# Performance work log

Hardware: AMD Instinct MI355X
Metric: run time of the kernel (lower is better)

The kernel has to match this reference:

```python
import jax, jax.numpy as jnp
from jax import lax
import numpy as np

N_QUBITS = 8
Q_DEPTH = 10
DIM = 256  # 2**8

# basis-state bit table; wire 0 = most-significant bit (PennyLane convention)
_bits = ((np.arange(DIM)[:, None] >> (N_QUBITS - 1 - np.arange(N_QUBITS))) & 1)
# phase layer: S on even wires (phase i), T on odd wires (phase e^{i pi/4})
_ph = np.where(np.arange(N_QUBITS) % 2 == 0, 1j, np.exp(1j * np.pi / 4))
_diag = np.prod(np.power(_ph[None, :], _bits), axis=1)
# entangling_layer_3 CZ pattern
_cz = np.ones(DIM)
for i, j in [(0, 1), (2, 3), (4, 5), (6, 7), (1, 2), (3, 4), (5, 6)]:
    _cz = _cz * ((-1.0) ** (_bits[:, i] * _bits[:, j]))
DIAG = jnp.asarray((_diag * _cz).astype(np.complex64))  # phase+CZ layer fused diagonal
ZSIGNS = jnp.asarray((1 - 2 * _bits).astype(np.float32))  # [256, 8] PauliZ eigenvalues
H_GATE = jnp.asarray((np.array([[1.0, 1.0], [1.0, -1.0]]) / np.sqrt(2.0)).astype(np.complex64))
X_GATE = jnp.asarray(np.array([[0.0, 1.0], [1.0, 0.0]]).astype(np.complex64))
EYE2 = jnp.eye(2, dtype=jnp.complex64)
BN_EPS = 1e-5


def apply_1q(state, U, w):
    """Apply 2x2 gate U on wire w; state: [B, 2,2,...,2]."""
    state = jnp.moveaxis(state, w + 1, -1)
    state = jnp.matmul(state, U.T)
    return jnp.moveaxis(state, -1, w + 1)


def quantum_net(features, q_params):
    """Batched statevector sim of quantum_net_3. features [B,256], q_params [80] -> [B,8]."""
    f = features / jnp.linalg.norm(features, axis=1, keepdims=True)
    state = f.astype(jnp.complex64).reshape((-1,) + (2,) * N_QUBITS)
    for w in range(N_QUBITS):
        state = apply_1q(state, H_GATE, w)
    qw = q_params.reshape(Q_DEPTH, N_QUBITS)
    for layer in range(Q_DEPTH):
        for w in range(N_QUBITS):
            t = qw[layer, w]
            c = jnp.cos(t / 2).astype(jnp.complex64)
            s = jnp.sin(t / 2).astype(jnp.complex64)
            U = c * EYE2 + (-1j) * s * X_GATE  # RX(t)
            state = apply_1q(state, U, w)
        flat = state.reshape(-1, DIM) * DIAG  # phase layer + CZ entangling (diagonal)
        state = flat.reshape((-1,) + (2,) * N_QUBITS)
    sv = state.reshape(-1, DIM)
    probs = sv.real ** 2 + sv.imag ** 2
    return probs @ ZSIGNS  # [B, 8] expval(PauliZ_i)


def conv2d(x, w, b):
    y = lax.conv_general_dilated(x, w, (1, 1), 'SAME', dimension_numbers=('NCHW', 'OIHW', 'NCHW'))
    return y + b[None, :, None, None]


def bn(x, gamma, beta, mean, var):  # eval-mode BatchNorm2d
    inv = gamma / jnp.sqrt(var + BN_EPS)
    return x * inv[None, :, None, None] + (beta - mean * inv)[None, :, None, None]


def maxpool2(x):
    return lax.reduce_window(x, -jnp.inf, lax.max, (1, 1, 2, 2), (1, 1, 2, 2), 'VALID')


def setup_inputs() -> dict:
    key = jax.random.key(0)
    ks = jax.random.split(key, 16)
    B = 1024
    return {
        'x': jax.random.normal(ks[0], (B, 1, 28, 28), dtype=jnp.float32),
        'conv1_w': 0.1 * jax.random.normal(ks[1], (32, 1, 3, 3), dtype=jnp.float32),
        'conv1_b': jnp.zeros((32,), jnp.float32),
        'bn1_gamma': jnp.ones((32,), jnp.float32),
        'bn1_beta': jnp.zeros((32,), jnp.float32),
        'bn1_mean': jnp.zeros((32,), jnp.float32),
        'bn1_var': jnp.ones((32,), jnp.float32),
        'conv2_w': 0.05 * jax.random.normal(ks[2], (64, 32, 3, 3), dtype=jnp.float32),
        'conv2_b': jnp.zeros((64,), jnp.float32),
        'bn2_gamma': jnp.ones((64,), jnp.float32),
        'bn2_beta': jnp.zeros((64,), jnp.float32),
        'bn2_mean': jnp.zeros((64,), jnp.float32),
        'bn2_var': jnp.ones((64,), jnp.float32),
        'fc_w': 0.01 * jax.random.normal(ks[3], (256, 64 * 7 * 7), dtype=jnp.float32),
        'fc_b': jnp.zeros((256,), jnp.float32),
        'q_params': 0.1 * jax.random.normal(ks[4], (Q_DEPTH * N_QUBITS,), dtype=jnp.float32),
        'p1_w': 0.01 * jax.random.normal(ks[5], (128, 8), dtype=jnp.float32),
        'p1_b': jnp.zeros((128,), jnp.float32),
        'p2_w': 0.01 * jax.random.normal(ks[6], (64, 128), dtype=jnp.float32),
        'p2_b': jnp.zeros((64,), jnp.float32),
        'p3_w': 0.01 * jax.random.normal(ks[7], (10, 64), dtype=jnp.float32),
        'p3_b': jnp.zeros((10,), jnp.float32),
    }


def reference(x, conv1_w, conv1_b, bn1_gamma, bn1_beta, bn1_mean, bn1_var,
              conv2_w, conv2_b, bn2_gamma, bn2_beta, bn2_mean, bn2_var,
              fc_w, fc_b, q_params, p1_w, p1_b, p2_w, p2_b, p3_w, p3_b):
    h = maxpool2(jax.nn.relu(bn(conv2d(x, conv1_w, conv1_b), bn1_gamma, bn1_beta, bn1_mean, bn1_var)))
    h = maxpool2(jax.nn.relu(bn(conv2d(h, conv2_w, conv2_b), bn2_gamma, bn2_beta, bn2_mean, bn2_var)))
    h = h.reshape(h.shape[0], -1)  # [B, 64*7*7]
    feats = jnp.tanh(h @ fc_w.T + fc_b)  # [B, 256]
    q = quantum_net(feats, q_params)  # [B, 8]
    z = jax.nn.relu(q @ p1_w.T + p1_b)  # dropout = identity (eval)
    z = jax.nn.relu(z @ p2_w.T + p2_b)
    return z @ p3_w.T + p3_b
```

## Files before the change

### kernel.cpp

```cpp
#include <hip/hip_runtime.h>
#include <math.h>


#define B_SZ 1024

#define OFF_FCWP   0
#define OFF_W2F    802816
#define OFF_W1T    821248
#define OFF_SC1    821536
#define OFF_SH1    821568
#define OFF_SC2    821600
#define OFF_SH2    821664
#define OFF_H1     821728
#define OFF_H2P    7244256

#define KSPLIT_FC 14
#define KCHUNK_FC 224

typedef __attribute__((ext_vector_type(8))) short s16x8;
typedef __attribute__((ext_vector_type(4))) float f32x4;

__constant__ float C_COS8[8] = {1.f, 0.70710678f, 0.f, -0.70710678f, -1.f, -0.70710678f, 0.f, 0.70710678f};
__constant__ float C_SIN8[8] = {0.f, 0.70710678f, 1.f, 0.70710678f, 0.f, -0.70710678f, -1.f, -0.70710678f};

__device__ __forceinline__ unsigned short bf16_rne(float f) {
  unsigned u = __float_as_uint(f);
  unsigned r = u + 0x7FFFu + ((u >> 16) & 1u);
  return (unsigned short)(r >> 16);
}
__device__ __forceinline__ int div14(int m) {
  return __float2int_rz((float)m * 0.07142858f);
}
__device__ __forceinline__ int swz16(int e) {
  return e ^ (((e >> 6) & 3) << 3);
}

__global__ __launch_bounds__(256) void prep_kernel(
    const float* __restrict__ fc_w, const float* __restrict__ c2w, const float* __restrict__ c1w,
    const float* __restrict__ bn1g, const float* __restrict__ bn1b, const float* __restrict__ bn1m,
    const float* __restrict__ bn1v, const float* __restrict__ c1b,
    const float* __restrict__ bn2g, const float* __restrict__ bn2b, const float* __restrict__ bn2m,
    const float* __restrict__ bn2v, const float* __restrict__ c2b,
    float* __restrict__ ws) {
  int g = blockIdx.x * 256 + threadIdx.x;

  {
    int j = g & 7, lane = (g >> 3) & 63, nt = (g >> 9) & 15, kg = g >> 13;
    int n = nt * 16 + (lane & 15);
    int k = kg * 32 + ((lane >> 4) & 3) * 8 + j;
    float v = fc_w[n * 3136 + (k & 63) * 49 + (k >> 6)];
    unsigned short hi = bf16_rne(v);
    unsigned short lo = bf16_rne(v - __uint_as_float((unsigned)hi << 16));
    unsigned short* us = (unsigned short*)ws;
    int base = ((kg * 16 + nt) * 2) * 512 + lane * 8 + j;
    us[base] = hi;
    us[base + 512] = lo;
  }

  if (g < 36864) {
    int j = g & 7, L = (g >> 3) & 63, rest = g >> 9;
    int h = rest & 1; rest >>= 1;
    int t = rest % 9, w = rest / 9;
    int occ = w * 16 + (L & 15);
    int ic  = (L >> 4) * 8 + j;
    float v = c2w[occ * 288 + ic * 9 + t];
    unsigned short hi = bf16_rne(v);
    unsigned short res = hi;
    if (h) res = bf16_rne(v - __uint_as_float((unsigned)hi << 16));
    ((unsigned short*)(ws + OFF_W2F))[g] = res;
  }
  if (g < 288) {
    ws[OFF_W1T + g] = c1w[(g & 31) * 9 + (g >> 5)];
  }
  if (g < 32) {
    float inv = bn1g[g] / sqrtf(bn1v[g] + 1e-5f);
    ws[OFF_SC1 + g] = inv;
    ws[OFF_SH1 + g] = c1b[g] * inv + bn1b[g] - bn1m[g] * inv;
  }
  if (g < 64) {
    float inv = bn2g[g] / sqrtf(bn2v[g] + 1e-5f);
    ws[OFF_SC2 + g] = inv;
    ws[OFF_SH2 + g] = c2b[g] * inv + bn2b[g] - bn2m[g] * inv;
  }
}

__global__ __launch_bounds__(256) void conv1_kernel(
    const float* __restrict__ x, const float* __restrict__ w1T,
    const float* __restrict__ sc1, const float* __restrict__ sh1,
    float* __restrict__ h1) {
  const int b = blockIdx.x, tid = threadIdx.x;
  __shared__ float xs[30][32];
  __shared__ float w1s[288];
  __shared__ float sc1s[32], sh1s[32];

  float4* xsf = (float4*)&xs[0][0];
  if (tid < 240) xsf[tid] = make_float4(0.f, 0.f, 0.f, 0.f);
  __syncthreads();
  const float* xb = x + b * 784;
  for (int i = tid; i < 784; i += 256) {
    int y = i / 28, c = i - y * 28;
    xs[y + 1][c + 1] = xb[i];
  }
  for (int i = tid; i < 288; i += 256) w1s[i] = w1T[i];
  if (tid < 32) { sc1s[tid] = sc1[tid]; sh1s[tid] = sh1[tid]; }
  __syncthreads();

  for (int t = tid; t < 448; t += 256) {
    const int oc = t & 31, py = t >> 5;
    float wv[9];
#pragma unroll
    for (int k = 0; k < 9; ++k) wv[k] = w1s[k * 32 + oc];
    float acc0[28], acc1[28];
#pragma unroll
    for (int j = 0; j < 28; ++j) { acc0[j] = 0.f; acc1[j] = 0.f; }
#pragma unroll
    for (int r = 0; r < 4; ++r) {
      const int pr = 2 * py + r;
      float row[32];
#pragma unroll
      for (int q = 0; q < 8; ++q) {
        float4 v = *(const float4*)&xs[pr][4 * q];
        row[4 * q] = v.x; row[4 * q + 1] = v.y; row[4 * q + 2] = v.z; row[4 * q + 3] = v.w;
      }
      if (r <= 2) {
#pragma unroll
        for (int kx = 0; kx < 3; ++kx) {
          const float w = wv[r * 3 + kx];
#pragma unroll
          for (int xx = 0; xx < 28; ++xx) acc0[xx] = fmaf(row[xx + kx], w, acc0[xx]);
        }
      }
      if (r >= 1) {
#pragma unroll
        for (int kx = 0; kx < 3; ++kx) {
          const float w = wv[(r - 1) * 3 + kx];
#pragma unroll
          for (int xx = 0; xx < 28; ++xx) acc1[xx] = fmaf(row[xx + kx], w, acc1[xx]);
        }
      }
    }
    const float sc = sc1s[oc], sh = sh1s[oc];
    float* dst = h1 + b * 6272 + oc * 196 + py * 14;
#pragma unroll
    for (int px = 0; px < 14; ++px) {
      float v0 = fmaxf(fmaf(acc0[2 * px], sc, sh), 0.f);
      float v1 = fmaxf(fmaf(acc0[2 * px + 1], sc, sh), 0.f);
      float v2 = fmaxf(fmaf(acc1[2 * px], sc, sh), 0.f);
      float v3 = fmaxf(fmaf(acc1[2 * px + 1], sc, sh), 0.f);
      dst[px] = fmaxf(fmaxf(v0, v1), fmaxf(v2, v3));
    }
  }
}

__global__ __launch_bounds__(256, 2) void conv2_kernel(
    const float* __restrict__ h1, const float* __restrict__ w2f_f,
    const float* __restrict__ sc2, const float* __restrict__ sh2,
    unsigned short* __restrict__ h2hi, unsigned short* __restrict__ h2lo) {
  const int b = blockIdx.x, tid = threadIdx.x;
  const int lane = tid & 63, w = tid >> 6;

  __shared__ unsigned char lds_raw[50176];
  unsigned short* tile_hi = (unsigned short*)lds_raw;
  unsigned short* tile_lo = (unsigned short*)(lds_raw + 17408);
  float* conv_out = (float*)lds_raw;

  const unsigned short* w2f = (const unsigned short*)w2f_f;
  s16x8 bf[9][2];
#pragma unroll
  for (int t = 0; t < 9; ++t)
#pragma unroll
    for (int h = 0; h < 2; ++h)
      bf[t][h] = *(const s16x8*)&w2f[(((w * 9 + t) * 2 + h) << 9) + lane * 8];

  {
    float4* z = (float4*)lds_raw;
    for (int i = tid; i < 2176; i += 256) z[i] = make_float4(0.f, 0.f, 0.f, 0.f);
  }
  __syncthreads();

  if (tid < 196) {
    const int y = div14(tid), x = tid - y * 14;
    const int sp = ((y + 1) * 16 + (x + 1)) * 32;
    const float* src = h1 + b * 6272 + tid;
#pragma unroll
    for (int c = 0; c < 4; ++c) {
      s16x8 hv, lv;
#pragma unroll
      for (int j = 0; j < 8; ++j) {
        float v = src[(c * 8 + j) * 196];
        unsigned short h16 = bf16_rne(v);
        hv[j] = (short)h16;
        lv[j] = (short)bf16_rne(v - __uint_as_float((unsigned)h16 << 16));
      }
      const int sw = swz16(sp + c * 8);
      *(s16x8*)&tile_hi[sw] = hv;
      *(s16x8*)&tile_lo[sw] = lv;
    }
  }
  __syncthreads();

  f32x4 acc[13];
#pragma unroll
  for (int i = 0; i < 13; ++i) acc[i] = (f32x4){0.f, 0.f, 0.f, 0.f};

  const int kg8 = (lane >> 4) * 8;
#pragma unroll
  for (int mt = 0; mt < 13; ++mt) {
    const int m = mt * 16 + (lane & 15);
    const int y = div14(m), x = m - y * 14;
    const int base = (y * 16 + x) * 32 + kg8;
#pragma unroll
    for (int dy = 0; dy < 3; ++dy) {
#pragma unroll
      for (int dx = 0; dx < 3; ++dx) {
        const int off = swz16(base + (dy * 16 + dx) * 32);
        s16x8 ah = *(s16x8*)&tile_hi[off];
        s16x8 al = *(s16x8*)&tile_lo[off];
        const int t = dy * 3 + dx;
        acc[mt] = __builtin_amdgcn_mfma_f32_16x16x32_bf16(ah, bf[t][0], acc[mt], 0, 0, 0);
        acc[mt] = __builtin_amdgcn_mfma_f32_16x16x32_bf16(ah, bf[t][1], acc[mt], 0, 0, 0);
        acc[mt] = __builtin_amdgcn_mfma_f32_16x16x32_bf16(al, bf[t][0], acc[mt], 0, 0, 0);
      }
    }
  }
  __syncthreads();

  const int oc = w * 16 + (lane & 15);
  const float sc = sc2[oc], sh = sh2[oc];
  float* cw = conv_out + w * 3136;
#pragma unroll
  for (int mt = 0; mt < 13; ++mt) {
#pragma unroll
    for (int r = 0; r < 4; ++r) {
      const int m = mt * 16 + (lane >> 4) * 4 + r;
      if (m < 196) cw[m * 16 + (lane & 15)] = fmaxf(fmaf(acc[mt][r], sc, sh), 0.f);
    }
  }
  __syncthreads();

#pragma unroll
  for (int i = 0; i < 13; ++i) {
    const int ps = i * 4 + (lane >> 4);
    if (ps < 49) {
      const int py = (ps * 37) >> 8, px = ps - py * 7;
      const int m00 = py * 28 + px * 2;
      const int c0 = m00 * 16 + (lane & 15);
      float v0 = cw[c0], v1 = cw[c0 + 16], v2 = cw[c0 + 224], v3 = cw[c0 + 240];
      float vm = fmaxf(fmaxf(v0, v1), fmaxf(v2, v3));
      unsigned short hv = bf16_rne(vm);
      const int idx = b * 3136 + ps * 64 + oc;
      h2hi[idx] = hv;
      h2lo[idx] = bf16_rne(vm - __uint_as_float((unsigned)hv << 16));
    }
  }
}

__global__ __launch_bounds__(256) void fc_mfma_kernel(
    const unsigned short* __restrict__ h2hi, const unsigned short* __restrict__ h2lo,
    const unsigned short* __restrict__ Bfrag, float* __restrict__ Part) {
  __shared__ unsigned short Bs[8192];
  const int tid = threadIdx.x;
  const int lane = tid & 63, w = tid >> 6;
  const int m0 = blockIdx.y * 64, nt0 = blockIdx.x * 8, z = blockIdx.z;
  const int kz = z * KCHUNK_FC;

  const int mrow = m0 + w * 16 + (lane & 15);
  const int kg8 = (lane >> 4) * 8;
  const unsigned short* arow_hi = h2hi + mrow * 3136;
  const unsigned short* arow_lo = h2lo + mrow * 3136;

  f32x4 acc[8];
#pragma unroll
  for (int i = 0; i < 8; ++i) acc[i] = (f32x4){0.f, 0.f, 0.f, 0.f};

  for (int c = 0; c < 7; ++c) {
    const int kg = (kz >> 5) + c;
    {
      const uint4* src = (const uint4*)(Bfrag + (size_t)(kg * 16 + nt0) * 1024);
      uint4* dst = (uint4*)Bs;
#pragma unroll
      for (int i = 0; i < 4; ++i) dst[tid + 256 * i] = src[tid + 256 * i];
    }
    __syncthreads();

    const int k0 = kz + c * 32;
    s16x8 ah = *(const s16x8*)(arow_hi + k0 + kg8);
    s16x8 al = *(const s16x8*)(arow_lo + k0 + kg8);
#pragma unroll
    for (int nf = 0; nf < 8; ++nf) {
      s16x8 bh = *(s16x8*)&Bs[(nf * 2 + 0) * 512 + lane * 8];
      s16x8 bl = *(s16x8*)&Bs[(nf * 2 + 1) * 512 + lane * 8];
      acc[nf] = __builtin_amdgcn_mfma_f32_16x16x32_bf16(ah, bh, acc[nf], 0, 0, 0);
      acc[nf] = __builtin_amdgcn_mfma_f32_16x16x32_bf16(ah, bl, acc[nf], 0, 0, 0);
      acc[nf] = __builtin_amdgcn_mfma_f32_16x16x32_bf16(al, bh, acc[nf], 0, 0, 0);
    }
    __syncthreads();
  }

  float* dst = Part + (size_t)z * 262144;
  const int mbase = m0 + w * 16 + (lane >> 4) * 4;
  const int nbase = nt0 * 16 + (lane & 15);
#pragma unroll
  for (int nf = 0; nf < 8; ++nf) {
#pragma unroll
    for (int r = 0; r < 4; ++r) {
      dst[(mbase + r) * 256 + nbase + nf * 16] = acc[nf][r];
    }
  }
}

__global__ __launch_bounds__(256) void quantum_kernel(
    const float* __restrict__ Part, const float* __restrict__ fc_b,
    const float* __restrict__ qp,
    const float* __restrict__ p1w, const float* __restrict__ p1b,
    const float* __restrict__ p2w, const float* __restrict__ p2b,
    const float* __restrict__ p3w, const float* __restrict__ p3b,
    float* __restrict__ out) {
  const int b = blockIdx.x, tid = threadIdx.x;
  __shared__ float2 buf[2][256];
  __shared__ float csl[160];
  __shared__ float part[4][8];
  __shared__ float qv[8];
  __shared__ float z1[128];
  __shared__ float z2s[64];

  if (tid < 80) {
    float t = 0.5f * qp[tid];
    csl[2 * tid] = cosf(t);
    csl[2 * tid + 1] = sinf(t);
  }

  float f = fc_b[tid];
#pragma unroll
  for (int z = 0; z < KSPLIT_FC; ++z) f += Part[z * 262144 + b * 256 + tid];
  f = tanhf(f);

  float ss = f * f;
#pragma unroll
  for (int off = 32; off >= 1; off >>= 1) ss += __shfl_xor(ss, off);
  const int lane = tid & 63, wid = tid >> 6;
  if (lane == 0) part[wid][0] = ss;
  __syncthreads();
  const float tot = part[0][0] + part[1][0] + part[2][0] + part[3][0];
  const float inv = 1.0f / sqrtf(tot);
  float re = f * inv, im = 0.f;

  const int k8 = (2 * __popc(tid & 0xAA) + __popc(tid & 0x55)) & 7;
  float dre = C_COS8[k8], dim_ = C_SIN8[k8];
  {
    const int i = tid;
    int par = ((i >> 7) & (i >> 6)) ^ ((i >> 5) & (i >> 4)) ^ ((i >> 3) & (i >> 2)) ^ ((i >> 1) & i)
            ^ ((i >> 6) & (i >> 5)) ^ ((i >> 4) & (i >> 3)) ^ ((i >> 2) & (i >> 1));
    if (par & 1) { dre = -dre; dim_ = -dim_; }
  }

  int cur = 0;
  const float RS = 0.70710678118654752f;

#pragma unroll
  for (int w = 0; w < 2; ++w) {
    const int m = 128 >> w;
    cur ^= 1;
    buf[cur][tid] = make_float2(re, im);
    __syncthreads();
    float2 p = buf[cur][tid ^ m];
    float sgn = (tid & m) ? -1.f : 1.f;
    re = fmaf(sgn, re, p.x) * RS;
    im = fmaf(sgn, im, p.y) * RS;
  }
#pragma unroll
  for (int w = 2; w < 8; ++w) {
    const int m = 1 << (7 - w);
    float pre = __shfl_xor(re, m);
    float pim = __shfl_xor(im, m);
    float sgn = (tid & m) ? -1.f : 1.f;
    re = fmaf(sgn, re, pre) * RS;
    im = fmaf(sgn, im, pim) * RS;
  }

  for (int layer = 0; layer < 10; ++layer) {
    const float* cs = &csl[16 * layer];
#pragma unroll
    for (int w = 0; w < 2; ++w) {
      const int m = 128 >> w;
      const float c = cs[2 * w], s = cs[2 * w + 1];
      cur ^= 1;
      buf[cur][tid] = make_float2(re, im);
      __syncthreads();
      float2 p = buf[cur][tid ^ m];
      float nre = fmaf(s, p.y, c * re);
      float nim = fmaf(-s, p.x, c * im);
      re = nre; im = nim;
    }
#pragma unroll
    for (int w = 2; w < 8; ++w) {
      const int m = 1 << (7 - w);
      const float c = cs[2 * w], s = cs[2 * w + 1];
      float pre = __shfl_xor(re, m);
      float pim = __shfl_xor(im, m);
      float nre = fmaf(s, pim, c * re);
      float nim = fmaf(-s, pre, c * im);
      if (w == 7) {
        float tre = nre * dre - nim * dim_;
        nim = fmaf(nre, dim_, nim * dre);
        nre = tre;
      }
      re = nre; im = nim;
    }
  }

  const float prb = re * re + im * im;
#pragma unroll
  for (int w = 0; w < 8; ++w) {
    float v = ((tid >> (7 - w)) & 1) ? -prb : prb;
#pragma unroll
    for (int off = 32; off >= 1; off >>= 1) v += __shfl_xor(v, off);
    if (lane == 0) part[wid][w] = v;
  }
  __syncthreads();
  if (tid < 8) qv[tid] = part[0][tid] + part[1][tid] + part[2][tid] + part[3][tid];
  __syncthreads();

  if (tid < 128) {
    float a = p1b[tid];
#pragma unroll
    for (int k = 0; k < 8; ++k) a = fmaf(qv[k], p1w[tid * 8 + k], a);
    z1[tid] = fmaxf(a, 0.f);
  }
  __syncthreads();
  if (tid < 64) {
    float a = p2b[tid];
#pragma unroll 16
    for (int k = 0; k < 128; ++k) a = fmaf(z1[k], p2w[tid * 128 + k], a);
    z2s[tid] = fmaxf(a, 0.f);
  }
  __syncthreads();
  if (tid < 10) {
    float a = p3b[tid];
#pragma unroll 16
    for (int k = 0; k < 64; ++k) a = fmaf(z2s[k], p3w[tid * 64 + k], a);
    out[b * 10 + tid] = a;
  }
}

extern "C" void kernel_launch(void* const* d_in, const int* in_sizes, int n_in,
                              void* d_out, int out_size, void* d_ws, size_t ws_size,
                              hipStream_t stream) {
  (void)in_sizes; (void)n_in; (void)out_size; (void)ws_size;
  const float* x    = (const float*)d_in[0];
  const float* c1w  = (const float*)d_in[1];
  const float* c1b  = (const float*)d_in[2];
  const float* bn1g = (const float*)d_in[3];
  const float* bn1b = (const float*)d_in[4];
  const float* bn1m = (const float*)d_in[5];
  const float* bn1v = (const float*)d_in[6];
  const float* c2w  = (const float*)d_in[7];
  const float* c2b  = (const float*)d_in[8];
  const float* bn2g = (const float*)d_in[9];
  const float* bn2b = (const float*)d_in[10];
  const float* bn2m = (const float*)d_in[11];
  const float* bn2v = (const float*)d_in[12];
  const float* fc_w = (const float*)d_in[13];
  const float* fc_b = (const float*)d_in[14];
  const float* qp   = (const float*)d_in[15];
  const float* p1w  = (const float*)d_in[16];
  const float* p1b  = (const float*)d_in[17];
  const float* p2w  = (const float*)d_in[18];
  const float* p2b  = (const float*)d_in[19];
  const float* p3w  = (const float*)d_in[20];
  const float* p3b  = (const float*)d_in[21];
  float* ws = (float*)d_ws;
  float* outp = (float*)d_out;

  unsigned short* h2hi = (unsigned short*)(ws + OFF_H2P);
  unsigned short* h2lo = h2hi + 3211264;
  const unsigned short* bfrag = (const unsigned short*)ws;

  prep_kernel<<<3136, 256, 0, stream>>>(fc_w, c2w, c1w,
                                        bn1g, bn1b, bn1m, bn1v, c1b,
                                        bn2g, bn2b, bn2m, bn2v, c2b, ws);
  conv1_kernel<<<B_SZ, 256, 0, stream>>>(x, ws + OFF_W1T, ws + OFF_SC1, ws + OFF_SH1, ws + OFF_H1);
  conv2_kernel<<<B_SZ, 256, 0, stream>>>(ws + OFF_H1, ws + OFF_W2F, ws + OFF_SC2, ws + OFF_SH2,
                                         h2hi, h2lo);
  fc_mfma_kernel<<<dim3(2, 16, KSPLIT_FC), 256, 0, stream>>>(h2hi, h2lo, bfrag, ws + OFF_H1);
  quantum_kernel<<<B_SZ, 256, 0, stream>>>(ws + OFF_H1, fc_b, qp, p1w, p1b, p2w, p2b, p3w, p3b, outp);
}
```

Baseline: 175.9 us.

## Fuse conv1 and conv2 into one kernel keeping pooled activations in LDS

```diff
diff --git a/kernel.cpp b/kernel.cpp
--- a/kernel.cpp
+++ b/kernel.cpp
@@ -84,22 +84,34 @@
   }
 }
 
-__global__ __launch_bounds__(256) void conv1_kernel(
+__global__ __launch_bounds__(256, 2) void conv12_kernel(
     const float* __restrict__ x, const float* __restrict__ w1T,
     const float* __restrict__ sc1, const float* __restrict__ sh1,
-    float* __restrict__ h1) {
+    const float* __restrict__ w2f_f,
+    const float* __restrict__ sc2, const float* __restrict__ sh2,
+    unsigned short* __restrict__ h2hi, unsigned short* __restrict__ h2lo) {
   const int b = blockIdx.x, tid = threadIdx.x;
-  __shared__ float xs[30][32];
-  __shared__ float w1s[288];
-  __shared__ float sc1s[32], sh1s[32];
-
-  float4* xsf = (float4*)&xs[0][0];
-  if (tid < 240) xsf[tid] = make_float4(0.f, 0.f, 0.f, 0.f);
-  __syncthreads();
+  const int lane = tid & 63, w = tid >> 6;
+
+  __shared__ unsigned char lds_raw[50176];
+  unsigned short* tile_hi = (unsigned short*)lds_raw;
+  unsigned short* tile_lo = (unsigned short*)(lds_raw + 17408);
+  float* xs  = (float*)(lds_raw + 34816);
+  float* w1s = (float*)(lds_raw + 38656);
+  float* sc1s = (float*)(lds_raw + 39808);
+  float* sh1s = sc1s + 32;
+  float* conv_out = (float*)lds_raw;
+
+  {
+    float4* z = (float4*)lds_raw;
+    for (int i = tid; i < 2416; i += 256) z[i] = make_float4(0.f, 0.f, 0.f, 0.f);
+  }
+  __syncthreads();
+
   const float* xb = x + b * 784;
   for (int i = tid; i < 784; i += 256) {
     int y = i / 28, c = i - y * 28;
-    xs[y + 1][c + 1] = xb[i];
+    xs[(y + 1) * 32 + (c + 1)] = xb[i];
   }
   for (int i = tid; i < 288; i += 256) w1s[i] = w1T[i];
   if (tid < 32) { sc1s[tid] = sc1[tid]; sh1s[tid] = sh1[tid]; }
@@ -119,50 +131,42 @@
       float row[32];
 #pragma unroll
       for (int q = 0; q < 8; ++q) {
-        float4 v = *(const float4*)&xs[pr][4 * q];
+        float4 v = *(const float4*)&xs[pr * 32 + 4 * q];
         row[4 * q] = v.x; row[4 * q + 1] = v.y; row[4 * q + 2] = v.z; row[4 * q + 3] = v.w;
       }
       if (r <= 2) {
 #pragma unroll
         for (int kx = 0; kx < 3; ++kx) {
-          const float w = wv[r * 3 + kx];
-#pragma unroll
-          for (int xx = 0; xx < 28; ++xx) acc0[xx] = fmaf(row[xx + kx], w, acc0[xx]);
+          const float w1v = wv[r * 3 + kx];
+#pragma unroll
+          for (int xx = 0; xx < 28; ++xx) acc0[xx] = fmaf(row[xx + kx], w1v, acc0[xx]);
         }
       }
       if (r >= 1) {
 #pragma unroll
         for (int kx = 0; kx < 3; ++kx) {
-          const float w = wv[(r - 1) * 3 + kx];
-#pragma unroll
-          for (int xx = 0; xx < 28; ++xx) acc1[xx] = fmaf(row[xx + kx], w, acc1[xx]);
+          const float w1v = wv[(r - 1) * 3 + kx];
+#pragma unroll
+          for (int xx = 0; xx < 28; ++xx) acc1[xx] = fmaf(row[xx + kx], w1v, acc1[xx]);
         }
       }
     }
     const float sc = sc1s[oc], sh = sh1s[oc];
-    float* dst = h1 + b * 6272 + oc * 196 + py * 14;
 #pragma unroll
     for (int px = 0; px < 14; ++px) {
       float v0 = fmaxf(fmaf(acc0[2 * px], sc, sh), 0.f);
       float v1 = fmaxf(fmaf(acc0[2 * px + 1], sc, sh), 0.f);
       float v2 = fmaxf(fmaf(acc1[2 * px], sc, sh), 0.f);
       float v3 = fmaxf(fmaf(acc1[2 * px + 1], sc, sh), 0.f);
-      dst[px] = fmaxf(fmaxf(v0, v1), fmaxf(v2, v3));
-    }
-  }
-}
-
-__global__ __launch_bounds__(256, 2) void conv2_kernel(
-    const float* __restrict__ h1, const float* __restrict__ w2f_f,
-    const float* __restrict__ sc2, const float* __restrict__ sh2,
-    unsigned short* __restrict__ h2hi, unsigned short* __restrict__ h2lo) {
-  const int b = blockIdx.x, tid = threadIdx.x;
-  const int lane = tid & 63, w = tid >> 6;
-
-  __shared__ unsigned char lds_raw[50176];
-  unsigned short* tile_hi = (unsigned short*)lds_raw;
-  unsigned short* tile_lo = (unsigned short*)(lds_raw + 17408);
-  float* conv_out = (float*)lds_raw;
+      float vm = fmaxf(fmaxf(v0, v1), fmaxf(v2, v3));
+      unsigned short hv = bf16_rne(vm);
+      unsigned short lv = bf16_rne(vm - __uint_as_float((unsigned)hv << 16));
+      const int e = swz16(((py + 1) * 16 + (px + 1)) * 32 + oc);
+      tile_hi[e] = hv;
+      tile_lo[e] = lv;
+    }
+  }
+  __syncthreads();
 
   const unsigned short* w2f = (const unsigned short*)w2f_f;
   s16x8 bf[9][2];
@@ -172,33 +176,6 @@
     for (int h = 0; h < 2; ++h)
       bf[t][h] = *(const s16x8*)&w2f[(((w * 9 + t) * 2 + h) << 9) + lane * 8];
 
-  {
-    float4* z = (float4*)lds_raw;
-    for (int i = tid; i < 2176; i += 256) z[i] = make_float4(0.f, 0.f, 0.f, 0.f);
-  }
-  __syncthreads();
-
-  if (tid < 196) {
-    const int y = div14(tid), x = tid - y * 14;
-    const int sp = ((y + 1) * 16 + (x + 1)) * 32;
-    const float* src = h1 + b * 6272 + tid;
-#pragma unroll
-    for (int c = 0; c < 4; ++c) {
-      s16x8 hv, lv;
-#pragma unroll
-      for (int j = 0; j < 8; ++j) {
-        float v = src[(c * 8 + j) * 196];
-        unsigned short h16 = bf16_rne(v);
-        hv[j] = (short)h16;
-        lv[j] = (short)bf16_rne(v - __uint_as_float((unsigned)h16 << 16));
-      }
-      const int sw = swz16(sp + c * 8);
-      *(s16x8*)&tile_hi[sw] = hv;
-      *(s16x8*)&tile_lo[sw] = lv;
-    }
-  }
-  __syncthreads();
-
   f32x4 acc[13];
 #pragma unroll
   for (int i = 0; i < 13; ++i) acc[i] = (f32x4){0.f, 0.f, 0.f, 0.f};
@@ -207,8 +184,8 @@
 #pragma unroll
   for (int mt = 0; mt < 13; ++mt) {
     const int m = mt * 16 + (lane & 15);
-    const int y = div14(m), x = m - y * 14;
-    const int base = (y * 16 + x) * 32 + kg8;
+    const int y = div14(m), xx = m - y * 14;
+    const int base = (y * 16 + xx) * 32 + kg8;
 #pragma unroll
     for (int dy = 0; dy < 3; ++dy) {
 #pragma unroll
@@ -479,9 +456,9 @@
   prep_kernel<<<3136, 256, 0, stream>>>(fc_w, c2w, c1w,
                                         bn1g, bn1b, bn1m, bn1v, c1b,
                                         bn2g, bn2b, bn2m, bn2v, c2b, ws);
-  conv1_kernel<<<B_SZ, 256, 0, stream>>>(x, ws + OFF_W1T, ws + OFF_SC1, ws + OFF_SH1, ws + OFF_H1);
-  conv2_kernel<<<B_SZ, 256, 0, stream>>>(ws + OFF_H1, ws + OFF_W2F, ws + OFF_SC2, ws + OFF_SH2,
-                                         h2hi, h2lo);
+  conv12_kernel<<<B_SZ, 256, 0, stream>>>(x, ws + OFF_W1T, ws + OFF_SC1, ws + OFF_SH1,
+                                          ws + OFF_W2F, ws + OFF_SC2, ws + OFF_SH2,
+                                          h2hi, h2lo);
   fc_mfma_kernel<<<dim3(2, 16, KSPLIT_FC), 256, 0, stream>>>(h2hi, h2lo, bfrag, ws + OFF_H1);
   quantum_kernel<<<B_SZ, 256, 0, stream>>>(ws + OFF_H1, fc_b, qp, p1w, p1b, p2w, p2b, p3w, p3b, outp);
 }
```

After: 166.6 us. 1.06x faster.
